# Kernel tuning notes

Hardware: AMD Instinct MI355X
Metric: run time of the kernel (lower is better)

## Reference

```python
import jax, jax.numpy as jnp
import numpy as np

D_MODEL = 768
EXPAND = 2
D_STATE = 128
HEADDIM = 64
D_CONV = 4
D_INNER = EXPAND * D_MODEL            # 1536
NHEADS = D_INNER // HEADDIM           # 24
CONV_DIM = D_INNER + 2 * D_STATE      # 1792
D_IN_PROJ = 2 * D_INNER + 2 * D_STATE + NHEADS  # 3352
EPS = 1e-5
BATCH, SEQLEN = 2, 2048


def silu(v):
    return v * jax.nn.sigmoid(v)


def mamba2(x, in_w, conv_w, conv_b, dt_bias, A_log, Dp, norm_w, out_w):
    # x: (b, l, d_model)
    b, l, _ = x.shape
    zxbcdt = x @ in_w.T                              # (b, l, d_in_proj)
    z = zxbcdt[..., :D_INNER]
    xBC = zxbcdt[..., D_INNER:D_INNER + CONV_DIM]
    dt = jax.nn.softplus(zxbcdt[..., D_INNER + CONV_DIM:] + dt_bias)  # (b, l, h)
    # causal depthwise conv1d, kernel D_CONV, left padding D_CONV-1
    pad = jnp.pad(xBC, ((0, 0), (D_CONV - 1, 0), (0, 0)))
    conv = conv_b
    for k in range(D_CONV):
        conv = conv + pad[:, k:k + l, :] * conv_w[:, k]
    xBC = silu(conv)
    xh = xBC[..., :D_INNER].reshape(b, l, NHEADS, HEADDIM)   # (b,l,h,p)
    Bm = xBC[..., D_INNER:D_INNER + D_STATE]                 # (b,l,n) ngroups=1
    Cm = xBC[..., D_INNER + D_STATE:]                        # (b,l,n)
    A = -jnp.exp(A_log)                                      # (h,)
    dA = jnp.exp(dt * A)                                     # (b,l,h)

    def step(h, inp):
        dA_t, dt_t, x_t, B_t, C_t = inp
        # h: (b, h, p, n)
        h = h * dA_t[:, :, None, None] + (dt_t[:, :, None] * x_t)[..., None] * B_t[:, None, None, :]
        y = jnp.einsum('bhpn,bn->bhp', h, C_t)
        return h, y

    h0 = jnp.zeros((b, NHEADS, HEADDIM, D_STATE), x.dtype)
    xs = (dA.transpose(1, 0, 2), dt.transpose(1, 0, 2), xh.transpose(1, 0, 2, 3),
          Bm.transpose(1, 0, 2), Cm.transpose(1, 0, 2))
    _, ys = jax.lax.scan(step, h0, xs)                       # (l,b,h,p)
    y = ys.transpose(1, 0, 2, 3) + Dp[None, None, :, None] * xh
    y = y.reshape(b, l, D_INNER)
    # RMSNormGated (norm_before_gate=False): rmsnorm(y * silu(z)) * weight
    y = y * silu(z)
    y = y * jax.lax.rsqrt(jnp.mean(jnp.square(y), axis=-1, keepdims=True) + EPS) * norm_w
    return y @ out_w.T


def setup_inputs() -> dict:
    key = jax.random.key(0)
    ks = jax.random.split(key, 9)
    s = 0.02
    return {
        'x': jax.random.normal(ks[0], (BATCH, SEQLEN, D_MODEL), jnp.float32),
        'in_proj_w': jax.random.normal(ks[1], (2, D_IN_PROJ, D_MODEL), jnp.float32) * s,
        'conv_w': jax.random.normal(ks[2], (2, CONV_DIM, D_CONV), jnp.float32) * 0.2,
        'conv_b': jax.random.normal(ks[3], (2, CONV_DIM), jnp.float32) * s,
        'dt_bias': jax.random.normal(ks[4], (2, NHEADS), jnp.float32) * 0.1,
        'A_log': jnp.log(jax.random.uniform(ks[5], (2, NHEADS), jnp.float32, 1.0, 16.0)),
        'D': jax.random.normal(ks[6], (2, NHEADS), jnp.float32) * 0.5 + 1.0,
        'norm_w': jnp.ones((2, D_INNER), jnp.float32),
        'out_proj_w': jax.random.normal(ks[7], (2, D_MODEL, D_INNER), jnp.float32) * s,
    }


def reference(x, in_proj_w, conv_w, conv_b, dt_bias, A_log, D, norm_w, out_proj_w):
    h_fwd = mamba2(x, in_proj_w[0], conv_w[0], conv_b[0], dt_bias[0], A_log[0], D[0], norm_w[0], out_proj_w[0])
    x_rev = jnp.flip(x, axis=1)
    h_bwd_rev = mamba2(x_rev, in_proj_w[1], conv_w[1], conv_b[1], dt_bias[1], A_log[1], D[1], norm_w[1], out_proj_w[1])
    return h_fwd + jnp.flip(h_bwd_rev, axis=1)
```

## Files before the change

### kernel.cpp

```cpp
#include <hip/hip_runtime.h>
#include <hip/hip_bf16.h>

typedef __attribute__((ext_vector_type(8))) short short8;
typedef __attribute__((ext_vector_type(4))) short bfx4;
typedef __attribute__((ext_vector_type(4))) float floatx4;

#define SEQ     2048
#define DMODEL  768
#define DINNER  1536
#define DSTATE  128
#define NH      24
#define CONVDIM 1792
#define NPROJ   3352
#define QCH     64
#define NCH     (SEQ / QCH)

__device__ inline float bf2f(short s) {
    return __uint_as_float(((unsigned)(unsigned short)s) << 16);
}
__device__ inline short f2bf(float f) {
    __hip_bfloat16 h = __float2bfloat16(f);
    return *reinterpret_cast<short*>(&h);
}
__device__ inline void gl_lds16(const void* g, void* l) {
    __builtin_amdgcn_global_load_lds((const __attribute__((address_space(1))) unsigned int*)g,
                                     (__attribute__((address_space(3))) unsigned int*)l, 16, 0, 0);
}

__global__ __launch_bounds__(256) void cvt3_kernel(const float* __restrict__ s1, __hip_bfloat16* __restrict__ d1, int n1,
                                                   const float* __restrict__ s2, __hip_bfloat16* __restrict__ d2, int n2,
                                                   const float* __restrict__ s3, __hip_bfloat16* __restrict__ d3, int n3) {
    int i = blockIdx.x * 256 + threadIdx.x;
    const float* src; __hip_bfloat16* dst; int idx;
    if (i < n1)                { src = s1; dst = d1; idx = i; }
    else if (i < n1 + n2)      { src = s2; dst = d2; idx = i - n1; }
    else if (i < n1 + n2 + n3) { src = s3; dst = d3; idx = i - n1 - n2; }
    else return;
    float4 v = *(const float4*)(src + (size_t)idx * 4);
    bfx4 o = { f2bf(v.x), f2bf(v.y), f2bf(v.z), f2bf(v.w) };
    *(bfx4*)((short*)dst + (size_t)idx * 4) = o;
}

__global__ __launch_bounds__(256) void gemm_in(const __hip_bfloat16* __restrict__ Abase,
                                               const __hip_bfloat16* __restrict__ Bbase, size_t bStride,
                                               __hip_bfloat16* __restrict__ Zb,
                                               __hip_bfloat16* __restrict__ Xb,
                                               float* __restrict__ DT,
                                               float* __restrict__ LA,
                                               const float* __restrict__ dtbias,
                                               const float* __restrict__ Alog,
                                               int N, int K) {
    __shared__ short As[2][32 * 64];
    __shared__ short Bs[2][64 * 64];
    __shared__ short Tr[32][136];
    int tid = threadIdx.x;
    int w = tid >> 6, lane = tid & 63;
    int q = lane >> 4, mm = lane & 15;
    int wm = w >> 1, wn = w & 1;
    int m0 = blockIdx.x * 64, n0 = blockIdx.y * 128;
    int dir = blockIdx.z;
    const short* Ag = (const short*)Abase;
    const short* Bg = (const short*)Bbase + (size_t)dir * bStride;
    int fA = dir;

    size_t aoff; int aldso;
    {
        int ln = w * 8 + (lane >> 3);
        int s  = lane & 7;
        int c  = s ^ (ln & 7);
        int row = (c < 4) ? ln : ln + 32;
        int ch  = (c < 4) ? c : (c ^ 4);
        int ar = m0 + row;
        if (fA) { int bb = ar >> 11, tt = ar & 2047; ar = (bb << 11) + (2047 - tt); }
        aoff = (size_t)ar * K + ch * 8;
        aldso = w * 1024;
    }
    size_t boff[2];
    int bldso[2];
#pragma unroll
    for (int j = 0; j < 2; j++) {
        int widx = w * 2 + j;
        int ln = widx * 8 + (lane >> 3);
        int s  = lane & 7;
        int c  = s ^ (ln & 7);
        int row = (c < 4) ? ln : ln + 64;
        int ch  = (c < 4) ? c : (c ^ 4);
        int br = n0 + row; if (br > N - 1) br = N - 1;
        boff[j] = (size_t)br * K + ch * 8;
        bldso[j] = widx * 1024;
    }

    floatx4 acc[8];
#pragma unroll
    for (int i = 0; i < 8; i++) acc[i] = (floatx4){0.f, 0.f, 0.f, 0.f};

    int niter = K / 32;
    auto stage = [&](int buf, int k0) {
        gl_lds16(Ag + aoff + k0, (char*)&As[buf][0] + aldso);
        gl_lds16(Bg + boff[0] + k0, (char*)&Bs[buf][0] + bldso[0]);
        gl_lds16(Bg + boff[1] + k0, (char*)&Bs[buf][0] + bldso[1]);
    };
    stage(0, 0);
    int slotA = (q ^ (mm & 7) ^ (wm << 2)) * 8;
    int slotB = (q ^ (mm & 7) ^ (wn << 2)) * 8;
    for (int it = 0; it < niter; it++) {
        __syncthreads();
        if (it + 1 < niter) stage((it + 1) & 1, (it + 1) * 32);
        const short* Ab = &As[it & 1][0];
        const short* Bb = &Bs[it & 1][0];
        short8 af[2], bfr[4];
#pragma unroll
        for (int mb = 0; mb < 2; mb++)
            af[mb] = *(const short8*)&Ab[(mb * 16 + mm) * 64 + slotA];
#pragma unroll
        for (int nb = 0; nb < 4; nb++)
            bfr[nb] = *(const short8*)&Bb[(nb * 16 + mm) * 64 + slotB];
#pragma unroll
        for (int mb = 0; mb < 2; mb++)
#pragma unroll
            for (int nb = 0; nb < 4; nb++)
                acc[mb * 4 + nb] = __builtin_amdgcn_mfma_f32_16x16x32_bf16(af[mb], bfr[nb], acc[mb * 4 + nb], 0, 0, 0);
    }

    __hip_bfloat16* Zb2 = Zb + (size_t)dir * 4096 * DINNER;
    __hip_bfloat16* Xb2 = Xb + (size_t)dir * 4096 * CONVDIM;

    if (n0 + 128 <= DINNER + CONVDIM) {
        short* dstBase; int ldd, c0;
        if (n0 < DINNER) { dstBase = (short*)Zb2; ldd = DINNER; c0 = n0; }
        else             { dstBase = (short*)Xb2; ldd = CONVDIM; c0 = n0 - DINNER; }
#pragma unroll
        for (int p = 0; p < 2; p++) {
            __syncthreads();
            if (wm == p) {
#pragma unroll
                for (int mb = 0; mb < 2; mb++)
#pragma unroll
                    for (int nb = 0; nb < 4; nb++)
#pragma unroll
                        for (int r = 0; r < 4; r++)
                            Tr[mb * 16 + q * 4 + r][wn * 64 + nb * 16 + mm] =
                                f2bf(acc[mb * 4 + nb][r]);
            }
            __syncthreads();
            int row = tid >> 3, c16 = (tid & 7) * 16;
            short8 v0 = *(const short8*)&Tr[row][c16];
            short8 v1 = *(const short8*)&Tr[row][c16 + 8];
            short* dp = dstBase + (size_t)(m0 + p * 32 + row) * ldd + c0 + c16;
            *(short8*)dp = v0;
            *(short8*)(dp + 8) = v1;
        }
        return;
    }

    float* DT2 = DT + (size_t)dir * 4096 * NH;
    float* LA2 = LA + (size_t)dir * 4096 * NH;
    const float* dtb2 = dtbias + dir * NH;
    const float* Al2  = Alog + dir * NH;
#pragma unroll
    for (int mb = 0; mb < 2; mb++) {
#pragma unroll
        for (int nb = 0; nb < 4; nb++) {
            int col = n0 + wn * 64 + nb * 16 + mm;
            if (col >= N) continue;
#pragma unroll
            for (int r = 0; r < 4; r++) {
                int rr = m0 + wm * 32 + mb * 16 + q * 4 + r;
                float v = acc[mb * 4 + nb][r];
                int hh = col - (DINNER + CONVDIM);
                float raw = v + dtb2[hh];
                float dtv = (raw > 20.f) ? raw : log1pf(__expf(raw));
                float Av  = -__expf(Al2[hh]);
                DT2[(size_t)rr * NH + hh] = dtv;
                LA2[(size_t)rr * NH + hh] = dtv * Av;
            }
        }
    }
}

__global__ __launch_bounds__(256) void gemm_out(const __hip_bfloat16* __restrict__ Abase, size_t aStride,
                                                const __hip_bfloat16* __restrict__ Bbase, size_t bStride,
                                                float* __restrict__ C,
                                                int N, int K, int zdiv) {
    __shared__ short As[2][32 * 64];
    __shared__ short Bs[2][64 * 64];
    int tid = threadIdx.x;
    int w = tid >> 6, lane = tid & 63;
    int q = lane >> 4, mm = lane & 15;
    int wm = w >> 1, wn = w & 1;
    int m0 = blockIdx.x * 64, n0 = blockIdx.y * 128;
    int z = blockIdx.z;
    int kl   = K / zdiv;
    int kbeg = z * kl;
    int niter = kl / 32;

    int aRow, aCh, aldso;
    {
        int ln = w * 8 + (lane >> 3);
        int s  = lane & 7;
        int c  = s ^ (ln & 7);
        aRow = (c < 4) ? ln : ln + 32;
        aCh  = (c < 4) ? c : (c ^ 4);
        aldso = w * 1024;
    }
    int bRow[2], bCh[2], bldso[2];
#pragma unroll
    for (int j = 0; j < 2; j++) {
        int widx = w * 2 + j;
        int ln = widx * 8 + (lane >> 3);
        int s  = lane & 7;
        int c  = s ^ (ln & 7);
        bRow[j] = (c < 4) ? ln : ln + 64;
        bCh[j]  = (c < 4) ? c : (c ^ 4);
        bldso[j] = widx * 1024;
    }

    floatx4 acc[8];
#pragma unroll
    for (int i = 0; i < 8; i++) acc[i] = (floatx4){0.f, 0.f, 0.f, 0.f};

    int slotA = (q ^ (mm & 7) ^ (wm << 2)) * 8;
    int slotB = (q ^ (mm & 7) ^ (wn << 2)) * 8;

    for (int d = 0; d < 2; d++) {
        const short* Ag = (const short*)Abase + (size_t)d * aStride;
        const short* Bg = (const short*)Bbase + (size_t)d * bStride;
        size_t aoff;
        {
            int ar = m0 + aRow;
            if (d) { int bb = ar >> 11, tt = ar & 2047; ar = (bb << 11) + (2047 - tt); }
            aoff = (size_t)ar * K + aCh * 8;
        }
        size_t boff[2];
#pragma unroll
        for (int j = 0; j < 2; j++) {
            int br = n0 + bRow[j]; if (br > N - 1) br = N - 1;
            boff[j] = (size_t)br * K + bCh[j] * 8;
        }
        auto stage = [&](int buf, int k0) {
            gl_lds16(Ag + aoff + kbeg + k0, (char*)&As[buf][0] + aldso);
            gl_lds16(Bg + boff[0] + kbeg + k0, (char*)&Bs[buf][0] + bldso[0]);
            gl_lds16(Bg + boff[1] + kbeg + k0, (char*)&Bs[buf][0] + bldso[1]);
        };
        stage(0, 0);
        for (int it = 0; it < niter; it++) {
            __syncthreads();
            if (it + 1 < niter) stage((it + 1) & 1, (it + 1) * 32);
            const short* Ab = &As[it & 1][0];
            const short* Bb = &Bs[it & 1][0];
            short8 af[2], bfr[4];
#pragma unroll
            for (int mb = 0; mb < 2; mb++)
                af[mb] = *(const short8*)&Ab[(mb * 16 + mm) * 64 + slotA];
#pragma unroll
            for (int nb = 0; nb < 4; nb++)
                bfr[nb] = *(const short8*)&Bb[(nb * 16 + mm) * 64 + slotB];
#pragma unroll
            for (int mb = 0; mb < 2; mb++)
#pragma unroll
                for (int nb = 0; nb < 4; nb++)
                    acc[mb * 4 + nb] = __builtin_amdgcn_mfma_f32_16x16x32_bf16(af[mb], bfr[nb], acc[mb * 4 + nb], 0, 0, 0);
        }
    }

    float* Cz = C + (size_t)z * 4096 * 768;
#pragma unroll
    for (int mb = 0; mb < 2; mb++)
#pragma unroll
        for (int nb = 0; nb < 4; nb++) {
            int col = n0 + wn * 64 + nb * 16 + mm;
#pragma unroll
            for (int r = 0; r < 4; r++) {
                int rr = m0 + wm * 32 + mb * 16 + q * 4 + r;
                Cz[(size_t)rr * 768 + col] = acc[mb * 4 + nb][r];
            }
        }
}

__global__ __launch_bounds__(256) void reduce2_kernel(const float* __restrict__ P, float* __restrict__ out) {
    int idx = blockIdx.x * 256 + threadIdx.x;
    const size_t sl = (size_t)4096 * 192;
    const float4* P4 = (const float4*)P;
    float4 a = P4[idx];
    float4 b = P4[sl + idx];
    float4 o = { a.x + b.x, a.y + b.y, a.z + b.z, a.w + b.w };
    ((float4*)out)[idx] = o;
}

__global__ __launch_bounds__(256) void conv_kernel(const __hip_bfloat16* __restrict__ Xb,
                                                   const float* __restrict__ conv_w,
                                                   const float* __restrict__ conv_b,
                                                   __hip_bfloat16* __restrict__ xh,
                                                   __hip_bfloat16* __restrict__ Bm,
                                                   __hip_bfloat16* __restrict__ Cm) {
    int db  = blockIdx.x >> 7;
    int dir = db >> 1;
    int t0  = (blockIdx.x & 127) * 16;
    int c8  = threadIdx.x * 8;
    if (c8 >= CONVDIM) return;

    float wk[4][8], bs[8];
#pragma unroll
    for (int j = 0; j < 8; j++) {
        bs[j] = conv_b[dir * CONVDIM + c8 + j];
#pragma unroll
        for (int k = 0; k < 4; k++) wk[k][j] = conv_w[((size_t)dir * CONVDIM + c8 + j) * 4 + k];
    }

    const short* xrow = (const short*)Xb + (size_t)db * SEQ * CONVDIM + c8;
    short8 win[4];
    const short8 zer = {0, 0, 0, 0, 0, 0, 0, 0};
#pragma unroll
    for (int k = 0; k < 3; k++) {
        int ts = t0 - 3 + k;
        win[k] = (ts >= 0) ? *(const short8*)(xrow + (size_t)ts * CONVDIM) : zer;
    }

    for (int tt = 0; tt < 16; tt++) {
        int t = t0 + tt;
        win[3] = *(const short8*)(xrow + (size_t)t * CONVDIM);
        short8 outv;
#pragma unroll
        for (int j = 0; j < 8; j++) {
            float acc = bs[j];
#pragma unroll
            for (int k = 0; k < 4; k++) acc += wk[k][j] * bf2f(win[k][j]);
            float sv = acc / (1.f + __expf(-acc));
            outv[j] = f2bf(sv);
        }
        if (c8 < DINNER)
            *(short8*)((short*)xh + (size_t)(db * SEQ + t) * DINNER + c8) = outv;
        else if (c8 < DINNER + DSTATE)
            *(short8*)((short*)Bm + (size_t)(db * SEQ + t) * DSTATE + (c8 - DINNER)) = outv;
        else
            *(short8*)((short*)Cm + (size_t)(db * SEQ + t) * DSTATE + (c8 - DINNER - DSTATE)) = outv;
        win[0] = win[1]; win[1] = win[2]; win[2] = win[3];
    }
}

__global__ __launch_bounds__(256) void ssd1_kernel(const __hip_bfloat16* __restrict__ XH,
                                                   const __hip_bfloat16* __restrict__ BMh,
                                                   const float* __restrict__ DT,
                                                   const float* __restrict__ LA,
                                                   short* __restrict__ SS,
                                                   float* __restrict__ CUM) {
    int blk = blockIdx.x;
    int ck = blk & 31;
    int dbh = blk >> 5;
    int hh = dbh % NH, db = dbh / NH;
    int base_row = db * SEQ + ck * QCH;

    __shared__ float cum_s[QCH], dt_s[QCH];
    __shared__ short Xt[64][72];
    __shared__ short Bt[128][72];

    int tid = threadIdx.x;
    int lane = tid & 63, w = tid >> 6;
    int q = lane >> 4, mm = lane & 15;

    if (tid < QCH) {
        float la  = LA[(size_t)(base_row + tid) * NH + hh];
        float dtv = DT[(size_t)(base_row + tid) * NH + hh];
        float cs = la;
#pragma unroll
        for (int d = 1; d < 64; d <<= 1) {
            float u = __shfl_up(cs, d);
            if (tid >= d) cs += u;
        }
        cum_s[tid] = cs;
        dt_s[tid] = dtv;
        CUM[(size_t)dbh * SEQ + ck * QCH + tid] = cs;
    }
    __syncthreads();
    float cumL = cum_s[QCH - 1];

    {
        int s2 = (tid & 31) * 2, pb = tid >> 5;
        float f0 = dt_s[s2]     * __expf(cumL - cum_s[s2]);
        float f1 = dt_s[s2 + 1] * __expf(cumL - cum_s[s2 + 1]);
        const short* r0 = (const short*)XH + (size_t)(base_row + s2) * DINNER + hh * 64 + pb * 8;
        const short* r1 = r0 + DINNER;
        short8 x0 = *(const short8*)r0;
        short8 x1 = *(const short8*)r1;
#pragma unroll
        for (int j = 0; j < 8; j++) {
            unsigned lo = (unsigned short)f2bf(f0 * bf2f(x0[j]));
            unsigned hi = (unsigned short)f2bf(f1 * bf2f(x1[j]));
            *(unsigned*)&Xt[pb * 8 + j][s2] = lo | (hi << 16);
        }
    }
    {
        int s2 = (tid & 31) * 2, nb = tid >> 5;
        const short* r0 = (const short*)BMh + (size_t)(base_row + s2) * DSTATE + nb * 16;
        const short* r1 = r0 + DSTATE;
        short8 b0a = *(const short8*)r0,  b0b = *(const short8*)(r0 + 8);
        short8 b1a = *(const short8*)r1,  b1b = *(const short8*)(r1 + 8);
#pragma unroll
        for (int j = 0; j < 8; j++) {
            *(unsigned*)&Bt[nb * 16 + j][s2] =
                (unsigned)(unsigned short)b0a[j] | ((unsigned)(unsigned short)b1a[j] << 16);
            *(unsigned*)&Bt[nb * 16 + 8 + j][s2] =
                (unsigned)(unsigned short)b0b[j] | ((unsigned)(unsigned short)b1b[j] << 16);
        }
    }
    __syncthreads();

    floatx4 acc[8];
#pragma unroll
    for (int i = 0; i < 8; i++) acc[i] = (floatx4){0.f, 0.f, 0.f, 0.f};
#pragma unroll
    for (int kk = 0; kk < 2; kk++) {
        short8 a = *(const short8*)&Xt[w * 16 + mm][kk * 32 + q * 8];
#pragma unroll
        for (int cb = 0; cb < 8; cb++) {
            short8 b = *(const short8*)&Bt[cb * 16 + mm][kk * 32 + q * 8];
            acc[cb] = __builtin_amdgcn_mfma_f32_16x16x32_bf16(a, b, acc[cb], 0, 0, 0);
        }
    }
    short* Sp = SS + (size_t)blk * 8192;
#pragma unroll
    for (int cb = 0; cb < 8; cb++)
#pragma unroll
        for (int r = 0; r < 4; r++)
            Sp[(w * 16 + q * 4 + r) * DSTATE + cb * 16 + mm] = f2bf(acc[cb][r]);
}

__global__ __launch_bounds__(256) void ssd2_kernel(const short* __restrict__ SS,
                                                   const float* __restrict__ CUM,
                                                   short* __restrict__ Hprev) {
    int blk = blockIdx.x;
    int dbh = blk >> 2, part = blk & 3;
    int off = part * 2048 + threadIdx.x * 8;
    size_t base = (size_t)dbh * NCH * 8192 + off;
    float h[8];
#pragma unroll
    for (int j = 0; j < 8; j++) h[j] = 0.f;
    for (int c = 0; c < NCH; c++) {
        float W = __expf(CUM[(size_t)dbh * SEQ + c * QCH + QCH - 1]);
        size_t p = base + (size_t)c * 8192;
        short8 s = *(const short8*)(SS + p);
        short8 o;
#pragma unroll
        for (int j = 0; j < 8; j++) o[j] = f2bf(h[j]);
        *(short8*)(Hprev + p) = o;
#pragma unroll
        for (int j = 0; j < 8; j++) h[j] = fmaf(h[j], W, bf2f(s[j]));
    }
}

__global__ __launch_bounds__(256) void ssd3_kernel(const __hip_bfloat16* __restrict__ XH,
                                                   const __hip_bfloat16* __restrict__ BMh,
                                                   const __hip_bfloat16* __restrict__ CMh,
                                                   const float* __restrict__ DT,
                                                   const float* __restrict__ CUM,
                                                   const short* __restrict__ Hprev,
                                                   __hip_bfloat16* __restrict__ Yb) {
    int blk = blockIdx.x;
    int ck = blk & 31;
    int dbh = blk >> 5;
    int hh = dbh % NH, db = dbh / NH;
    int base_row = db * SEQ + ck * QCH;

    __shared__ float cum_s[QCH], dt_s[QCH];
    __shared__ short Ct[64][136];
    __shared__ short G[64][72];
    __shared__ short Xt[64][72];

    int tid = threadIdx.x;
    int lane = tid & 63, w = tid >> 6;
    int q = lane >> 4, mm = lane & 15;

    if (tid < QCH) {
        cum_s[tid] = CUM[(size_t)dbh * SEQ + ck * QCH + tid];
        dt_s[tid]  = DT[(size_t)(base_row + tid) * NH + hh];
    }

    const short* Cg = (const short*)CMh + (size_t)base_row * DSTATE;
    const short* Bg = (const short*)BMh + (size_t)base_row * DSTATE;
    floatx4 P[4];
#pragma unroll
    for (int i = 0; i < 4; i++) P[i] = (floatx4){0.f, 0.f, 0.f, 0.f};
#pragma unroll
    for (int kk = 0; kk < 4; kk++) {
        short8 a = *(const short8*)(Cg + (size_t)(w * 16 + mm) * DSTATE + kk * 32 + q * 8);
#pragma unroll
        for (int cb = 0; cb < 4; cb++) {
            short8 b = *(const short8*)(Bg + (size_t)(cb * 16 + mm) * DSTATE + kk * 32 + q * 8);
            P[cb] = __builtin_amdgcn_mfma_f32_16x16x32_bf16(a, b, P[cb], 0, 0, 0);
        }
    }
    __syncthreads();

    {
        int t = tid & 63, nb4 = tid >> 6;
        float wt = __expf(cum_s[t]);
        const short* src = Cg + (size_t)t * DSTATE + nb4 * 32;
#pragma unroll
        for (int u = 0; u < 2; u++) {
            short8 v = *(const short8*)(src + u * 16);
            short8 v2 = *(const short8*)(src + u * 16 + 8);
#pragma unroll
            for (int j = 0; j < 4; j++) {
                unsigned lo = (unsigned short)f2bf(wt * bf2f(v[2 * j]));
                unsigned hi = (unsigned short)f2bf(wt * bf2f(v[2 * j + 1]));
                *(unsigned*)&Ct[t][nb4 * 32 + u * 16 + 2 * j] = lo | (hi << 16);
                lo = (unsigned short)f2bf(wt * bf2f(v2[2 * j]));
                hi = (unsigned short)f2bf(wt * bf2f(v2[2 * j + 1]));
                *(unsigned*)&Ct[t][nb4 * 32 + u * 16 + 8 + 2 * j] = lo | (hi << 16);
            }
        }
    }
    {
        int s2 = (tid & 31) * 2, pb = tid >> 5;
        const short* r0 = (const short*)XH + (size_t)(base_row + s2) * DINNER + hh * 64 + pb * 8;
        const short* r1 = r0 + DINNER;
        short8 x0 = *(const short8*)r0;
        short8 x1 = *(const short8*)r1;
#pragma unroll
        for (int j = 0; j < 8; j++) {
            *(unsigned*)&Xt[pb * 8 + j][s2] =
                (unsigned)(unsigned short)x0[j] | ((unsigned)(unsigned short)x1[j] << 16);
        }
    }
#pragma unroll
    for (int cb = 0; cb < 4; cb++) {
#pragma unroll
        for (int r = 0; r < 4; r++) {
            int t = w * 16 + q * 4 + r;
            int s = cb * 16 + mm;
            float g = (s <= t) ? P[cb][r] * __expf(cum_s[t] - cum_s[s]) * dt_s[s] : 0.f;
            G[t][s] = f2bf(g);
        }
    }
    __syncthreads();

    floatx4 Y[4];
#pragma unroll
    for (int i = 0; i < 4; i++) Y[i] = (floatx4){0.f, 0.f, 0.f, 0.f};
#pragma unroll
    for (int kk = 0; kk < 2; kk++) {
        short8 a = *(const short8*)&G[w * 16 + mm][kk * 32 + q * 8];
#pragma unroll
        for (int cb = 0; cb < 4; cb++) {
            short8 b = *(const short8*)&Xt[cb * 16 + mm][kk * 32 + q * 8];
            Y[cb] = __builtin_amdgcn_mfma_f32_16x16x32_bf16(a, b, Y[cb], 0, 0, 0);
        }
    }
    const short* Hc = Hprev + (size_t)blk * 8192;
#pragma unroll
    for (int kk = 0; kk < 4; kk++) {
        short8 a = *(const short8*)&Ct[w * 16 + mm][kk * 32 + q * 8];
#pragma unroll
        for (int cb = 0; cb < 4; cb++) {
            short8 b = *(const short8*)(Hc + (size_t)(cb * 16 + mm) * DSTATE + kk * 32 + q * 8);
            Y[cb] = __builtin_amdgcn_mfma_f32_16x16x32_bf16(a, b, Y[cb], 0, 0, 0);
        }
    }
#pragma unroll
    for (int cb = 0; cb < 4; cb++)
#pragma unroll
        for (int r = 0; r < 4; r++)
            Yb[(size_t)(base_row + w * 16 + q * 4 + r) * DINNER + hh * 64 + cb * 16 + mm] =
                __float2bfloat16(Y[cb][r]);
}

__global__ __launch_bounds__(192) void gate_kernel(const __hip_bfloat16* __restrict__ Yb,
                                                   const __hip_bfloat16* __restrict__ xh,
                                                   const __hip_bfloat16* __restrict__ Zb,
                                                   const float* __restrict__ Dp,
                                                   const float* __restrict__ norm_w,
                                                   __hip_bfloat16* __restrict__ A2) {
    int row = blockIdx.x;
    int dir = row >> 12;
    int c8 = threadIdx.x * 8;
    int hd = c8 >> 6;
    const short* yr = (const short*)Yb + (size_t)row * DINNER + c8;
    const short* xr = (const short*)xh + (size_t)row * DINNER + c8;
    const short* zr = (const short*)Zb + (size_t)row * DINNER + c8;

    short8 y8 = *(const short8*)yr;
    short8 x8 = *(const short8*)xr;
    short8 z8 = *(const short8*)zr;
    float Dv = Dp[dir * NH + hd];

    float vals[8];
    float ss = 0.f;
#pragma unroll
    for (int j = 0; j < 8; j++) {
        float v = bf2f(y8[j]) + Dv * bf2f(x8[j]);
        float z = bf2f(z8[j]);
        v *= z / (1.f + __expf(-z));
        vals[j] = v;
        ss += v * v;
    }
#pragma unroll
    for (int off = 32; off; off >>= 1) ss += __shfl_down(ss, off);
    __shared__ float ls[3];
    if ((threadIdx.x & 63) == 0) ls[threadIdx.x >> 6] = ss;
    __syncthreads();
    float tot = ls[0] + ls[1] + ls[2];
    float scale = rsqrtf(tot / (float)DINNER + 1e-5f);

    const float* nw = norm_w + dir * DINNER + c8;
    short8 o;
#pragma unroll
    for (int j = 0; j < 8; j++) o[j] = f2bf(vals[j] * scale * nw[j]);
    *(short8*)((short*)A2 + (size_t)row * DINNER + c8) = o;
}

extern "C" void kernel_launch(void* const* d_in, const int* in_sizes, int n_in,
                              void* d_out, int out_size, void* d_ws, size_t ws_size,
                              hipStream_t stream) {
    const float* x        = (const float*)d_in[0];
    const float* in_w     = (const float*)d_in[1];
    const float* conv_w   = (const float*)d_in[2];
    const float* conv_b   = (const float*)d_in[3];
    const float* dt_bias  = (const float*)d_in[4];
    const float* A_log    = (const float*)d_in[5];
    const float* Dp       = (const float*)d_in[6];
    const float* norm_w   = (const float*)d_in[7];
    const float* out_w    = (const float*)d_in[8];
    float* out = (float*)d_out;

    const size_t szW2 = (size_t)2 * DMODEL * DINNER * 2;
    const size_t szZ  = (size_t)8192 * DINNER * 2;
    const size_t szXH = (size_t)8192 * DINNER * 2;
    const size_t szBM = (size_t)8192 * DSTATE * 2;
    const size_t szCM = szBM;
    const size_t szDT = (size_t)8192 * NH * 4;
    const size_t szLA = szDT;
    const size_t szA1 = (size_t)4096 * DMODEL * 2;
    const size_t szW1 = (size_t)2 * NPROJ * DMODEL * 2;
    const size_t szXB = (size_t)8192 * CONVDIM * 2;
    const size_t szYb = (size_t)8192 * DINNER * 2;
    const size_t szSS = (size_t)96 * NCH * 8192 * 2;
    const size_t szCp = (size_t)2 * 4096 * 768 * 4;
    const size_t szRa = szA1 + szW1 + szXB;
    size_t szR = szRa;
    if (szR < szYb) szR = szYb;
    if (szR < szSS) szR = szSS;
    if (szR < szCp) szR = szCp;
    const size_t szHp = szSS;
    const size_t szCU = (size_t)96 * SEQ * 4;

    char* ws = (char*)d_ws;
    size_t off = 0;
    auto alloc = [&](size_t bytes) { char* p = ws + off; off += (bytes + 255) & ~(size_t)255; return p; };

    __hip_bfloat16* W2 = (__hip_bfloat16*)alloc(szW2);
    __hip_bfloat16* Z  = (__hip_bfloat16*)alloc(szZ);
    __hip_bfloat16* XH = (__hip_bfloat16*)alloc(szXH);
    __hip_bfloat16* BM = (__hip_bfloat16*)alloc(szBM);
    __hip_bfloat16* CM = (__hip_bfloat16*)alloc(szCM);
    float* DT = (float*)alloc(szDT);
    float* LA = (float*)alloc(szLA);
    char*  R  = (char*)alloc(szR);
    __hip_bfloat16* A1  = (__hip_bfloat16*)R;
    __hip_bfloat16* W1  = (__hip_bfloat16*)(R + szA1);
    __hip_bfloat16* XBC = (__hip_bfloat16*)(R + szA1 + szW1);
    short* SS = (short*)R;
    __hip_bfloat16* Yb = (__hip_bfloat16*)R;
    float* Cpart = (float*)R;

    short* Hp = (short*)alloc(szHp);
    float* CU = (float*)alloc(szCU);
    if (off > ws_size) return;

    int n1 = 2 * NPROJ * DMODEL / 4;
    int n2 = 2 * DMODEL * DINNER / 4;
    int n3 = 4096 * DMODEL / 4;
    cvt3_kernel<<<(n1 + n2 + n3 + 255) / 256, 256, 0, stream>>>(in_w, W1, n1, out_w, W2, n2, x, A1, n3);

    {
        dim3 grid(4096 / 64, (NPROJ + 127) / 128, 2);
        gemm_in<<<grid, 256, 0, stream>>>(A1,
                                          W1, (size_t)NPROJ * DMODEL,
                                          Z, XBC, DT, LA, dt_bias, A_log,
                                          NPROJ, DMODEL);
    }

    conv_kernel<<<4 * 128, 256, 0, stream>>>(XBC, conv_w, conv_b, XH, BM, CM);

    ssd1_kernel<<<4 * NH * NCH, 256, 0, stream>>>(XH, BM, DT, LA, SS, CU);
    ssd2_kernel<<<4 * NH * 4, 256, 0, stream>>>(SS, CU, Hp);
    ssd3_kernel<<<4 * NH * NCH, 256, 0, stream>>>(XH, BM, CM, DT, CU, Hp, Yb);

    gate_kernel<<<2 * 4096, 192, 0, stream>>>(Yb, XH, Z, Dp, norm_w, Z);

    {
        dim3 grid(4096 / 64, DMODEL / 128, 2);
        gemm_out<<<grid, 256, 0, stream>>>(Z, (size_t)4096 * DINNER,
                                           W2, (size_t)DMODEL * DINNER,
                                           Cpart,
                                           DMODEL, DINNER, 2);
    }
    reduce2_kernel<<<4096 * 192 / 256, 256, 0, stream>>>(Cpart, out);
}
```

Measured before the change: 348.3 us.

## Fuse causal depthwise conv and SiLU into the input-projection GEMM epilogue

Blocks of the input GEMM that produce xBC columns also compute a 16-row halo tile with extra MFMAs, so each block holds the three preceding timesteps. The block then applies the 4-tap causal conv and SiLU in its epilogue and writes XH/BM/CM directly. This removes the separate conv kernel and the round trip of the XBC intermediate through global memory. In exchange those blocks do redundant halo MFMAs, use more LDS (extra P and Ax buffers), which may lower occupancy, and have a heavier epilogue.

```diff
diff --git a/kernel.cpp b/kernel.cpp
--- a/kernel.cpp
+++ b/kernel.cpp
@@ -44,15 +44,21 @@
 __global__ __launch_bounds__(256) void gemm_in(const __hip_bfloat16* __restrict__ Abase,
                                                const __hip_bfloat16* __restrict__ Bbase, size_t bStride,
                                                __hip_bfloat16* __restrict__ Zb,
-                                               __hip_bfloat16* __restrict__ Xb,
+                                               __hip_bfloat16* __restrict__ XHp,
+                                               __hip_bfloat16* __restrict__ BMp,
+                                               __hip_bfloat16* __restrict__ CMp,
                                                float* __restrict__ DT,
                                                float* __restrict__ LA,
                                                const float* __restrict__ dtbias,
                                                const float* __restrict__ Alog,
+                                               const float* __restrict__ convw,
+                                               const float* __restrict__ convb,
                                                int N, int K) {
     __shared__ short As[2][32 * 64];
     __shared__ short Bs[2][64 * 64];
+    __shared__ short Ax[2][512];
     __shared__ short Tr[32][136];
+    __shared__ short P[67][136];
     int tid = threadIdx.x;
     int w = tid >> 6, lane = tid & 63;
     int q = lane >> 4, mm = lane & 15;
@@ -62,6 +68,7 @@
     const short* Ag = (const short*)Abase;
     const short* Bg = (const short*)Bbase + (size_t)dir * bStride;
     int fA = dir;
+    bool doX = (n0 >= DINNER) && (n0 + 128 <= DINNER + CONVDIM);
 
     size_t aoff; int aldso;
     {
@@ -74,6 +81,18 @@
         if (fA) { int bb = ar >> 11, tt = ar & 2047; ar = (bb << 11) + (2047 - tt); }
         aoff = (size_t)ar * K + ch * 8;
         aldso = w * 1024;
+    }
+    size_t aoffx = 0;
+    {
+        int lnx = lane >> 3;
+        int s   = lane & 7;
+        int c   = s ^ lnx;
+        int row = (c < 4) ? lnx : lnx + 8;
+        int ch  = (c < 4) ? c : (c ^ 4);
+        int ar  = m0 - 16 + row;
+        if (ar < 0) ar = 0;
+        if (fA) { int bb = ar >> 11, tt = ar & 2047; ar = (bb << 11) + (2047 - tt); }
+        aoffx = (size_t)ar * K + ch * 8;
     }
     size_t boff[2];
     int bldso[2];
@@ -90,19 +109,23 @@
         bldso[j] = widx * 1024;
     }
 
-    floatx4 acc[8];
+    floatx4 acc[8], accx[4];
 #pragma unroll
     for (int i = 0; i < 8; i++) acc[i] = (floatx4){0.f, 0.f, 0.f, 0.f};
+#pragma unroll
+    for (int i = 0; i < 4; i++) accx[i] = (floatx4){0.f, 0.f, 0.f, 0.f};
 
     int niter = K / 32;
     auto stage = [&](int buf, int k0) {
         gl_lds16(Ag + aoff + k0, (char*)&As[buf][0] + aldso);
         gl_lds16(Bg + boff[0] + k0, (char*)&Bs[buf][0] + bldso[0]);
         gl_lds16(Bg + boff[1] + k0, (char*)&Bs[buf][0] + bldso[1]);
+        if (doX && w == 0) gl_lds16(Ag + aoffx + k0, (char*)&Ax[buf][0]);
     };
     stage(0, 0);
     int slotA = (q ^ (mm & 7) ^ (wm << 2)) * 8;
     int slotB = (q ^ (mm & 7) ^ (wn << 2)) * 8;
+    int slotX = (mm & 7) * 64 + (q ^ ((mm >> 3) << 2) ^ (mm & 7)) * 8;
     for (int it = 0; it < niter; it++) {
         __syncthreads();
         if (it + 1 < niter) stage((it + 1) & 1, (it + 1) * 32);
@@ -120,15 +143,75 @@
 #pragma unroll
             for (int nb = 0; nb < 4; nb++)
                 acc[mb * 4 + nb] = __builtin_amdgcn_mfma_f32_16x16x32_bf16(af[mb], bfr[nb], acc[mb * 4 + nb], 0, 0, 0);
+        if (doX && wm == 0) {
+            short8 afx = *(const short8*)&Ax[it & 1][slotX];
+#pragma unroll
+            for (int nb = 0; nb < 4; nb++)
+                accx[nb] = __builtin_amdgcn_mfma_f32_16x16x32_bf16(afx, bfr[nb], accx[nb], 0, 0, 0);
+        }
     }
 
     __hip_bfloat16* Zb2 = Zb + (size_t)dir * 4096 * DINNER;
-    __hip_bfloat16* Xb2 = Xb + (size_t)dir * 4096 * CONVDIM;
-
-    if (n0 + 128 <= DINNER + CONVDIM) {
-        short* dstBase; int ldd, c0;
-        if (n0 < DINNER) { dstBase = (short*)Zb2; ldd = DINNER; c0 = n0; }
-        else             { dstBase = (short*)Xb2; ldd = CONVDIM; c0 = n0 - DINNER; }
+
+    if (doX) {
+        __syncthreads();
+#pragma unroll
+        for (int mb = 0; mb < 2; mb++)
+#pragma unroll
+            for (int nb = 0; nb < 4; nb++)
+#pragma unroll
+                for (int r = 0; r < 4; r++)
+                    P[3 + wm * 32 + mb * 16 + q * 4 + r][wn * 64 + nb * 16 + mm] =
+                        f2bf(acc[mb * 4 + nb][r]);
+        if (wm == 0 && q == 3) {
+#pragma unroll
+            for (int nb = 0; nb < 4; nb++)
+#pragma unroll
+                for (int r = 1; r < 4; r++)
+                    P[r - 1][wn * 64 + nb * 16 + mm] = f2bf(accx[nb][r]);
+        }
+        __syncthreads();
+
+        int cc0 = n0 - DINNER;
+        short* dst; int ldd, colofs;
+        if (cc0 < DINNER)      { dst = (short*)(XHp + (size_t)dir * 4096 * DINNER); ldd = DINNER; colofs = cc0; }
+        else if (cc0 < DINNER + DSTATE) { dst = (short*)(BMp + (size_t)dir * 4096 * DSTATE); ldd = DSTATE; colofs = cc0 - DINNER; }
+        else                   { dst = (short*)(CMp + (size_t)dir * 4096 * DSTATE); ldd = DSTATE; colofs = cc0 - DINNER - DSTATE; }
+
+        int cg = tid & 15;
+        int rb = tid >> 4;
+        float wk[4][8], bs[8];
+#pragma unroll
+        for (int j = 0; j < 8; j++) {
+            int cc = cc0 + cg * 8 + j;
+            bs[j] = convb[dir * CONVDIM + cc];
+#pragma unroll
+            for (int k = 0; k < 4; k++) wk[k][j] = convw[((size_t)dir * CONVDIM + cc) * 4 + k];
+        }
+        int tbase = m0 & 2047;
+#pragma unroll
+        for (int jj = 0; jj < 4; jj++) {
+            int lt = rb * 4 + jj;
+            int tg = tbase + lt;
+            short8 outv;
+#pragma unroll
+            for (int j = 0; j < 8; j++) {
+                float a = bs[j];
+#pragma unroll
+                for (int k = 0; k < 4; k++) {
+                    if (tg - 3 + k >= 0)
+                        a += wk[k][j] * bf2f(P[lt + k][cg * 8 + j]);
+                }
+                float sv = a / (1.f + __expf(-a));
+                outv[j] = f2bf(sv);
+            }
+            *(short8*)(dst + (size_t)(m0 + lt) * ldd + colofs + cg * 8) = outv;
+        }
+        return;
+    }
+
+    if (n0 + 128 <= DINNER) {
+        short* dstBase = (short*)Zb2; int ldd = DINNER; int c0 = n0;
 #pragma unroll
         for (int p = 0; p < 2; p++) {
             __syncthreads();
@@ -287,57 +370,6 @@
     ((float4*)out)[idx] = o;
 }
 
-__global__ __launch_bounds__(256) void conv_kernel(const __hip_bfloat16* __restrict__ Xb,
-                                                   const float* __restrict__ conv_w,
-                                                   const float* __restrict__ conv_b,
-                                                   __hip_bfloat16* __restrict__ xh,
-                                                   __hip_bfloat16* __restrict__ Bm,
-                                                   __hip_bfloat16* __restrict__ Cm) {
-    int db  = blockIdx.x >> 7;
-    int dir = db >> 1;
-    int t0  = (blockIdx.x & 127) * 16;
-    int c8  = threadIdx.x * 8;
-    if (c8 >= CONVDIM) return;
-
-    float wk[4][8], bs[8];
-#pragma unroll
-    for (int j = 0; j < 8; j++) {
-        bs[j] = conv_b[dir * CONVDIM + c8 + j];
-#pragma unroll
-        for (int k = 0; k < 4; k++) wk[k][j] = conv_w[((size_t)dir * CONVDIM + c8 + j) * 4 + k];
-    }
-
-    const short* xrow = (const short*)Xb + (size_t)db * SEQ * CONVDIM + c8;
-    short8 win[4];
-    const short8 zer = {0, 0, 0, 0, 0, 0, 0, 0};
-#pragma unroll
-    for (int k = 0; k < 3; k++) {
-        int ts = t0 - 3 + k;
-        win[k] = (ts >= 0) ? *(const short8*)(xrow + (size_t)ts * CONVDIM) : zer;
-    }
-
-    for (int tt = 0; tt < 16; tt++) {
-        int t = t0 + tt;
-        win[3] = *(const short8*)(xrow + (size_t)t * CONVDIM);
-        short8 outv;
-#pragma unroll
-        for (int j = 0; j < 8; j++) {
-            float acc = bs[j];
-#pragma unroll
-            for (int k = 0; k < 4; k++) acc += wk[k][j] * bf2f(win[k][j]);
-            float sv = acc / (1.f + __expf(-acc));
-            outv[j] = f2bf(sv);
-        }
-        if (c8 < DINNER)
-            *(short8*)((short*)xh + (size_t)(db * SEQ + t) * DINNER + c8) = outv;
-        else if (c8 < DINNER + DSTATE)
-            *(short8*)((short*)Bm + (size_t)(db * SEQ + t) * DSTATE + (c8 - DINNER)) = outv;
-        else
-            *(short8*)((short*)Cm + (size_t)(db * SEQ + t) * DSTATE + (c8 - DINNER - DSTATE)) = outv;
-        win[0] = win[1]; win[1] = win[2]; win[2] = win[3];
-    }
-}
-
 __global__ __launch_bounds__(256) void ssd1_kernel(const __hip_bfloat16* __restrict__ XH,
                                                    const __hip_bfloat16* __restrict__ BMh,
                                                    const float* __restrict__ DT,
@@ -631,11 +663,10 @@
     const size_t szLA = szDT;
     const size_t szA1 = (size_t)4096 * DMODEL * 2;
     const size_t szW1 = (size_t)2 * NPROJ * DMODEL * 2;
-    const size_t szXB = (size_t)8192 * CONVDIM * 2;
     const size_t szYb = (size_t)8192 * DINNER * 2;
     const size_t szSS = (size_t)96 * NCH * 8192 * 2;
     const size_t szCp = (size_t)2 * 4096 * 768 * 4;
-    const size_t szRa = szA1 + szW1 + szXB;
+    const size_t szRa = szA1 + szW1;
     size_t szR = szRa;
     if (szR < szYb) szR = szYb;
     if (szR < szSS) szR = szSS;
@@ -657,7 +688,6 @@
     char*  R  = (char*)alloc(szR);
     __hip_bfloat16* A1  = (__hip_bfloat16*)R;
     __hip_bfloat16* W1  = (__hip_bfloat16*)(R + szA1);
-    __hip_bfloat16* XBC = (__hip_bfloat16*)(R + szA1 + szW1);
     short* SS = (short*)R;
     __hip_bfloat16* Yb = (__hip_bfloat16*)R;
     float* Cpart = (float*)R;
@@ -675,11 +705,10 @@
         dim3 grid(4096 / 64, (NPROJ + 127) / 128, 2);
         gemm_in<<<grid, 256, 0, stream>>>(A1,
                                           W1, (size_t)NPROJ * DMODEL,
-                                          Z, XBC, DT, LA, dt_bias, A_log,
+                                          Z, XH, BM, CM, DT, LA, dt_bias, A_log,
+                                          conv_w, conv_b,
                                           NPROJ, DMODEL);
     }
-
-    conv_kernel<<<4 * 128, 256, 0, stream>>>(XBC, conv_w, conv_b, XH, BM, CM);
 
     ssd1_kernel<<<4 * NH * NCH, 256, 0, stream>>>(XH, BM, DT, LA, SS, CU);
     ssd2_kernel<<<4 * NH * 4, 256, 0, stream>>>(SS, CU, Hp);
```

Measured after the change: 354.6 us. Within noise of the previous version (+1.8%).
